# Kernel optimization log

Measured on AMD Instinct MI355X. Metric: run time of the kernel, lower is better.

## Reference

```python
import jax, jax.numpy as jnp
import numpy as np

B, N, D, H = 4, 2048, 1024, 16
DH = D // H


def setup_inputs() -> dict:
    key = jax.random.key(0)
    k_x, k_q, k_k, k_v, k_o = jax.random.split(key, 5)
    s = 1.0 / np.sqrt(D)
    return {
        "x": jax.random.normal(k_x, (B, N, D), dtype=jnp.float32),
        "mask": jnp.ones((B, N), dtype=bool),
        "Wq": jax.random.normal(k_q, (D, D), dtype=jnp.float32) * s,
        "Wk": jax.random.normal(k_k, (D, D), dtype=jnp.float32) * s,
        "Wv": jax.random.normal(k_v, (D, D), dtype=jnp.float32) * s,
        "Wo": jax.random.normal(k_o, (D, D), dtype=jnp.float32) * s,
    }


def reference(x, mask, Wq, Wk, Wv, Wo):
    # nn.Linear(bias=False): y = x @ W.T ; weights stored [out, in]
    q = jnp.einsum("bnd,ed->bne", x, Wq)
    k = jnp.einsum("bnd,ed->bne", x, Wk)
    v = jnp.einsum("bnd,ed->bne", x, Wv)
    # split heads: [b, n, d] -> [b, h, n, dh]
    def split(t):
        return t.reshape(B, N, H, DH).transpose(0, 2, 1, 3)
    q, k, v = split(q), split(k), split(v)
    # naive scaled dot-product attention (mask is dead code in the source)
    scores = jnp.einsum("bhnd,bhmd->bhnm", q, k) / jnp.sqrt(jnp.float32(DH))
    attn = jax.nn.softmax(scores, axis=-1)
    out = jnp.einsum("bhnm,bhmd->bhnd", attn, v)  # [b, h, n, dh]
    # merge heads: [b, h, n, dh] -> [b, n, d]
    out = out.transpose(0, 2, 1, 3).reshape(B, N, D)
    return jnp.einsum("bnd,ed->bne", out, Wo)
```

## Files before the change

### kernel.cpp

```cpp
#include <hip/hip_runtime.h>
#include <math.h>

constexpr int Bc  = 4;
constexpr int Nc  = 2048;
constexpr int Dc  = 1024;
constexpr int Hc  = 16;
constexpr int DHc = 64;
constexpr int Mrows = Bc * Nc;

typedef unsigned short ushortT;
typedef __attribute__((ext_vector_type(8))) short bf16x8;
typedef __attribute__((ext_vector_type(4))) unsigned short u16x4;
typedef __attribute__((ext_vector_type(4))) float f32x4;

#define QSCALE 0.18033688011112043f

#define GLD_LDS16(g, l)                                                        \
  __builtin_amdgcn_global_load_lds(                                            \
      (const __attribute__((address_space(1))) void*)(g),                      \
      (__attribute__((address_space(3))) void*)(l), 16, 0, 0)

__device__ inline ushortT f2bf(float f) {
  unsigned int u = __float_as_uint(f);
  u += 0x7fffu + ((u >> 16) & 1u);
  return (ushortT)(u >> 16);
}

__device__ inline float fexp2(float x) { return __builtin_amdgcn_exp2f(x); }

__global__ __launch_bounds__(256) void cvt_kernel(
    const float* __restrict__ x, const float* __restrict__ wq,
    const float* __restrict__ wk, const float* __restrict__ wv,
    const float* __restrict__ wo, ushortT* __restrict__ dst) {
  const int g = blockIdx.x * 256 + threadIdx.x;
  const float* src;
  size_t soff, doff;
  if (g < 2097152) {
    src = x;
    soff = (size_t)g * 4;
    doff = soff;
  } else {
    const int t = g - 2097152;
    const int w = t >> 18;
    const int off = t & 262143;
    src = (w == 0) ? wq : (w == 1) ? wk : (w == 2) ? wv : wo;
    soff = (size_t)off * 4;
    doff = 8388608u + (size_t)w * 1048576u + (size_t)off * 4;
  }
  float4 v = *(const float4*)(src + soff);
  ushort4 o = make_ushort4(f2bf(v.x), f2bf(v.y), f2bf(v.z), f2bf(v.w));
  *(ushort4*)(dst + doff) = o;
}

template <int QKV>
__global__ __launch_bounds__(256) void mfma_gemm(const ushortT* __restrict__ A,
                                                 const ushortT* __restrict__ W0,
                                                 void* __restrict__ C0) {
  __shared__ ushortT As[2][128 * 32];
  __shared__ ushortT Bs[2][128 * 32];

  const int tid = threadIdx.x;
  const int wave = tid >> 6, lane = tid & 63;
  const int quad = lane >> 4, lrow = lane & 15;

  const int gx = gridDim.x;
  const int nwg = gx * gridDim.y;
  const int orig = blockIdx.y * gx + blockIdx.x;
  const int swz = (orig & 7) * (nwg >> 3) + (orig >> 3);
  const int bx = swz % gx, by = swz / gx;

  const int wsel = QKV ? (bx >> 3) : 0;
  const int e0 = QKV ? ((bx & 7) * 128) : (bx * 128);
  const int m0 = by * 128;
  const ushortT* Wp = W0 + (size_t)wsel * (Dc * Dc);
  const float oscale = (QKV && wsel == 0) ? QSCALE : 1.0f;

  const ushortT* ag = A  + (size_t)(m0 + wave * 32 + (lane >> 2)) * Dc + (lane & 3) * 8;
  const ushortT* bg = Wp + (size_t)(e0 + wave * 32 + (lane >> 2)) * Dc + (lane & 3) * 8;
  const int lbase = wave * 1024 + lane * 8;

  f32x4 acc[4][4];
#pragma unroll
  for (int i = 0; i < 4; ++i)
#pragma unroll
    for (int j = 0; j < 4; ++j) acc[i][j] = (f32x4){0.f, 0.f, 0.f, 0.f};

  const int wm = (wave >> 1) * 64, wn = (wave & 1) * 64;

  for (int k0 = 0; k0 < Dc; k0 += 64) {
    __syncthreads();
#pragma unroll
    for (int p = 0; p < 2; ++p) {
      GLD_LDS16(ag + p * 32, &As[p][lbase]);
      GLD_LDS16(ag + p * 32 + 16 * Dc, &As[p][lbase + 512]);
      GLD_LDS16(bg + p * 32, &Bs[p][lbase]);
      GLD_LDS16(bg + p * 32 + 16 * Dc, &Bs[p][lbase + 512]);
    }
    ag += 64;
    bg += 64;
    __syncthreads();

#pragma unroll
    for (int p = 0; p < 2; ++p) {
      bf16x8 af[4], bf[4];
#pragma unroll
      for (int mt = 0; mt < 4; ++mt)
        af[mt] = *(const bf16x8*)(&As[p][(wm + mt * 16 + lrow) * 32 + quad * 8]);
#pragma unroll
      for (int nt = 0; nt < 4; ++nt)
        bf[nt] = *(const bf16x8*)(&Bs[p][(wn + nt * 16 + lrow) * 32 + quad * 8]);
      __builtin_amdgcn_s_setprio(1);
#pragma unroll
      for (int mt = 0; mt < 4; ++mt)
#pragma unroll
        for (int nt = 0; nt < 4; ++nt)
          acc[mt][nt] = __builtin_amdgcn_mfma_f32_16x16x32_bf16(
              af[mt], bf[nt], acc[mt][nt], 0, 0, 0);
      __builtin_amdgcn_s_setprio(0);
    }
  }

#pragma unroll
  for (int mt = 0; mt < 4; ++mt) {
#pragma unroll
    for (int nt = 0; nt < 4; ++nt) {
#pragma unroll
      for (int r = 0; r < 4; ++r) {
        const int m = m0 + wm + mt * 16 + quad * 4 + r;
        const int e = e0 + wn + nt * 16 + lrow;
        const float v = acc[mt][nt][r] * oscale;
        if (QKV) {
          const int b = m >> 11, n = m & 2047;
          const int h = e >> 6, dh = e & 63;
          ushortT* C = (ushortT*)C0 + (size_t)wsel * ((size_t)Mrows * Dc);
          C[(((size_t)(b * Hc + h)) * Nc + n) * DHc + dh] = f2bf(v);
        } else {
          ((float*)C0)[(size_t)m * Dc + e] = v;
        }
      }
    }
  }
}

__global__ __launch_bounds__(256, 2) void attn_mfma(const ushortT* __restrict__ Q,
                                                    const ushortT* __restrict__ K,
                                                    const ushortT* __restrict__ V,
                                                    ushortT* __restrict__ O) {
  __shared__ ushortT smemA[256 * 72];
  __shared__ ushortT Ks[2][64 * 64];
  __shared__ ushortT Vt[2][64 * 72];

  const int tid = threadIdx.x;
  const int wave = tid >> 6, lane = tid & 63;
  const int quad = lane >> 4, lrow = lane & 15;
  const int bh = blockIdx.y;
  const int q0 = blockIdx.x * 256;

  const ushortT* qg = Q + (size_t)bh * Nc * DHc;
  const ushortT* kg = K + (size_t)bh * Nc * DHc;
  const ushortT* vg = V + (size_t)bh * Nc * DHc;

  const int ksw = (lane & 3) ^ ((lane >> 3) & 3);
  const int krd = (lrow >> 1) & 3;

  const int kq = tid & 15;
  const int dhg = (tid >> 4) * 4;

#pragma unroll
  for (int c = 0; c < 2; ++c)
#pragma unroll
    for (int rh = 0; rh < 4; ++rh) {
      const int row = wave * 64 + rh * 16;
      GLD_LDS16(qg + (size_t)(q0 + row + (lane >> 2)) * DHc + c * 32 + (lane & 3) * 8,
                smemA + (c * 256 + row) * 32 + lane * 8);
    }
#pragma unroll
  for (int i = 0; i < 2; ++i) {
    const int cid = wave * 2 + i;
    const int c = cid & 1, kb = (cid >> 1) * 16;
    GLD_LDS16(kg + (size_t)(kb + (lane >> 2)) * DHc + c * 32 + ksw * 8,
              &Ks[0][(c * 64 + kb) * 32 + lane * 8]);
  }
  u16x4 vreg[4];
#pragma unroll
  for (int g = 0; g < 4; ++g)
    vreg[g] = *(const u16x4*)(vg + (size_t)(kq + 16 * g) * DHc + dhg);

  __syncthreads();

  bf16x8 af_q[4][2];
#pragma unroll
  for (int mt = 0; mt < 4; ++mt)
#pragma unroll
    for (int ks = 0; ks < 2; ++ks)
      af_q[mt][ks] = *(const bf16x8*)(smemA +
          ((ks * 256 + wave * 64 + mt * 16 + lrow) * 32 + quad * 8));

  {
    ushortT tmp[4][4];
#pragma unroll
    for (int g = 0; g < 4; ++g)
#pragma unroll
      for (int d = 0; d < 4; ++d) tmp[d][g] = vreg[g][d];
#pragma unroll
    for (int d = 0; d < 4; ++d)
      *(u16x4*)(&Vt[0][(dhg + d) * 72 + kq * 4]) = *(const u16x4*)tmp[d];
  }
  __syncthreads();

  f32x4 o_acc[4][4];
#pragma unroll
  for (int mt = 0; mt < 4; ++mt)
#pragma unroll
    for (int nt = 0; nt < 4; ++nt) o_acc[mt][nt] = (f32x4){0.f, 0.f, 0.f, 0.f};
  float l_i[16];
#pragma unroll
  for (int i = 0; i < 16; ++i) l_i[i] = 0.f;

  for (int k0 = 0; k0 < Nc; k0 += 64) {
    const int cur = (k0 >> 6) & 1, nxt = cur ^ 1;
    const bool pref = (k0 + 64 < Nc);

    if (pref) {
#pragma unroll
      for (int i = 0; i < 2; ++i) {
        const int cid = wave * 2 + i;
        const int c = cid & 1, kb = (cid >> 1) * 16;
        GLD_LDS16(kg + (size_t)(k0 + 64 + kb + (lane >> 2)) * DHc + c * 32 + ksw * 8,
                  &Ks[nxt][(c * 64 + kb) * 32 + lane * 8]);
      }
#pragma unroll
      for (int g = 0; g < 4; ++g)
        vreg[g] = *(const u16x4*)(vg + (size_t)(k0 + 64 + kq + 16 * g) * DHc + dhg);
    }

    bf16x8 bf_k[4][2];
#pragma unroll
    for (int nt = 0; nt < 4; ++nt)
#pragma unroll
      for (int ks = 0; ks < 2; ++ks)
        bf_k[nt][ks] = *(const bf16x8*)(
            &Ks[cur][(ks * 64 + nt * 16 + lrow) * 32 + (quad ^ krd) * 8]);

    f32x4 s_acc[4][4];
    __builtin_amdgcn_s_setprio(1);
#pragma unroll
    for (int mt = 0; mt < 4; ++mt)
#pragma unroll
      for (int nt = 0; nt < 4; ++nt) {
        s_acc[mt][nt] = (f32x4){0.f, 0.f, 0.f, 0.f};
#pragma unroll
        for (int ks = 0; ks < 2; ++ks)
          s_acc[mt][nt] = __builtin_amdgcn_mfma_f32_16x16x32_bf16(
              af_q[mt][ks], bf_k[nt][ks], s_acc[mt][nt], 0, 0, 0);
      }
    __builtin_amdgcn_s_setprio(0);

#pragma unroll
    for (int mt = 0; mt < 4; ++mt) {
#pragma unroll
      for (int r = 0; r < 4; ++r) {
        const float p0 = fexp2(s_acc[mt][0][r]);
        const float p1 = fexp2(s_acc[mt][1][r]);
        const float p2 = fexp2(s_acc[mt][2][r]);
        const float p3 = fexp2(s_acc[mt][3][r]);
        l_i[mt * 4 + r] += (p0 + p1) + (p2 + p3);
        const unsigned pk01 = __builtin_amdgcn_perm(
            __float_as_uint(p1), __float_as_uint(p0), 0x07060302u);
        const unsigned pk23 = __builtin_amdgcn_perm(
            __float_as_uint(p3), __float_as_uint(p2), 0x07060302u);
        const int row = wave * 64 + mt * 16 + quad * 4 + r;
        *(uint2*)(smemA + row * 72 + lrow * 4) = make_uint2(pk01, pk23);
      }
    }
    asm volatile("s_waitcnt lgkmcnt(0)" ::: "memory");

    bf16x8 af_p[4][2], bf_v[4][2];
#pragma unroll
    for (int mt = 0; mt < 4; ++mt)
#pragma unroll
      for (int ks = 0; ks < 2; ++ks)
        af_p[mt][ks] = *(const bf16x8*)(smemA +
            (wave * 64 + mt * 16 + lrow) * 72 + ks * 32 + quad * 8);
#pragma unroll
    for (int nt = 0; nt < 4; ++nt)
#pragma unroll
      for (int ks = 0; ks < 2; ++ks)
        bf_v[nt][ks] = *(const bf16x8*)(
            &Vt[cur][(nt * 16 + lrow) * 72 + ks * 32 + quad * 8]);
    __builtin_amdgcn_s_setprio(1);
#pragma unroll
    for (int mt = 0; mt < 4; ++mt)
#pragma unroll
      for (int nt = 0; nt < 4; ++nt)
#pragma unroll
        for (int ks = 0; ks < 2; ++ks)
          o_acc[mt][nt] = __builtin_amdgcn_mfma_f32_16x16x32_bf16(
              af_p[mt][ks], bf_v[nt][ks], o_acc[mt][nt], 0, 0, 0);
    __builtin_amdgcn_s_setprio(0);

    if (pref) {
      ushortT tmp[4][4];
#pragma unroll
      for (int g = 0; g < 4; ++g)
#pragma unroll
        for (int d = 0; d < 4; ++d) tmp[d][g] = vreg[g][d];
#pragma unroll
      for (int d = 0; d < 4; ++d)
        *(u16x4*)(&Vt[nxt][(dhg + d) * 72 + kq * 4]) = *(const u16x4*)tmp[d];
    }

    __syncthreads();
  }

#pragma unroll
  for (int i = 0; i < 16; ++i) {
    float s = l_i[i];
#pragma unroll
    for (int off = 8; off >= 1; off >>= 1) s += __shfl_xor(s, off, 16);
    l_i[i] = s;
  }

  const int b = bh / Hc, h = bh % Hc;
#pragma unroll
  for (int mt = 0; mt < 4; ++mt) {
#pragma unroll
    for (int r = 0; r < 4; ++r) {
      const float inv_l = 1.0f / l_i[mt * 4 + r];
      const int n = q0 + wave * 64 + mt * 16 + quad * 4 + r;
      const size_t base = ((size_t)b * Nc + n) * Dc + h * DHc;
#pragma unroll
      for (int nt = 0; nt < 4; ++nt)
        O[base + nt * 16 + lrow] = f2bf(o_acc[mt][nt][r] * inv_l);
    }
  }
}

extern "C" void kernel_launch(void* const* d_in, const int* in_sizes, int n_in,
                              void* d_out, int out_size, void* d_ws,
                              size_t ws_size, hipStream_t stream) {
  const float* x  = (const float*)d_in[0];
  const float* Wq = (const float*)d_in[2];
  const float* Wk = (const float*)d_in[3];
  const float* Wv = (const float*)d_in[4];
  const float* Wo = (const float*)d_in[5];

  ushortT* ws16 = (ushortT*)d_ws;
  ushortT* xb   = ws16;
  ushortT* wqb  = xb + (size_t)Mrows * Dc;
  ushortT* qkvb = wqb + 4 * (size_t)Dc * Dc;
  ushortT* qb   = qkvb;
  ushortT* kb   = qb + (size_t)Mrows * Dc;
  ushortT* vb   = kb + (size_t)Mrows * Dc;
  ushortT* aob  = vb + (size_t)Mrows * Dc;
  ushortT* wob  = wqb + 3 * (size_t)Dc * Dc;

  dim3 blk(256);
  hipLaunchKernelGGL(cvt_kernel, dim3(12288), blk, 0, stream, x, Wq, Wk, Wv, Wo,
                     ws16);

  hipLaunchKernelGGL((mfma_gemm<1>), dim3(24, Mrows / 128), blk, 0, stream, xb,
                     wqb, (void*)qkvb);

  hipLaunchKernelGGL(attn_mfma, dim3(Nc / 256, Bc * Hc), blk, 0, stream, qb,
                     kb, vb, aob);

  hipLaunchKernelGGL((mfma_gemm<0>), dim3(8, Mrows / 128), blk, 0, stream, aob,
                     wob, d_out);
}
```

Baseline: 297.6 us.

## Software-pipeline attention loop so next-tile QK^T overlaps current softmax and PV

Restructures the attention main loop into a two-stage software pipeline. The QK^T MFMAs for tile t+1 are issued while the exp/pack and PV MFMAs for tile t are in flight, using ping-pong score registers and a K prefetch two tiles ahead. V goes to a single-buffered LDS tile, which needs an extra barrier per iteration, and the setprio hints are dropped in both the GEMM and attention kernels. The aim is to hide exp and LDS latency behind matrix work, at the cost of more live registers (two score sets), which could cause spills or lower occupancy.

Result: slower. 524.6 us (+76.2%).

```diff
diff --git a/kernel.cpp b/kernel.cpp
--- a/kernel.cpp
+++ b/kernel.cpp
@@ -109,14 +109,12 @@
 #pragma unroll
       for (int nt = 0; nt < 4; ++nt)
         bf[nt] = *(const bf16x8*)(&Bs[p][(wn + nt * 16 + lrow) * 32 + quad * 8]);
-      __builtin_amdgcn_s_setprio(1);
 #pragma unroll
       for (int mt = 0; mt < 4; ++mt)
 #pragma unroll
         for (int nt = 0; nt < 4; ++nt)
           acc[mt][nt] = __builtin_amdgcn_mfma_f32_16x16x32_bf16(
               af[mt], bf[nt], acc[mt][nt], 0, 0, 0);
-      __builtin_amdgcn_s_setprio(0);
     }
   }
 
@@ -148,7 +146,7 @@
                                                     ushortT* __restrict__ O) {
   __shared__ ushortT smemA[256 * 72];
   __shared__ ushortT Ks[2][64 * 64];
-  __shared__ ushortT Vt[2][64 * 72];
+  __shared__ ushortT Vt[64 * 72];
 
   const int tid = threadIdx.x;
   const int wave = tid >> 6, lane = tid & 63;
@@ -204,10 +202,23 @@
       for (int d = 0; d < 4; ++d) tmp[d][g] = vreg[g][d];
 #pragma unroll
     for (int d = 0; d < 4; ++d)
-      *(u16x4*)(&Vt[0][(dhg + d) * 72 + kq * 4]) = *(const u16x4*)tmp[d];
-  }
+      *(u16x4*)(&Vt[(dhg + d) * 72 + kq * 4]) = *(const u16x4*)tmp[d];
+  }
+
+#pragma unroll
+  for (int g = 0; g < 4; ++g)
+    vreg[g] = *(const u16x4*)(vg + (size_t)(64 + kq + 16 * g) * DHc + dhg);
+#pragma unroll
+  for (int i = 0; i < 2; ++i) {
+    const int cid = wave * 2 + i;
+    const int c = cid & 1, kb = (cid >> 1) * 16;
+    GLD_LDS16(kg + (size_t)(64 + kb + (lane >> 2)) * DHc + c * 32 + ksw * 8,
+              &Ks[1][(c * 64 + kb) * 32 + lane * 8]);
+  }
+
   __syncthreads();
 
+  f32x4 sA[4][4], sB[4][4];
   f32x4 o_acc[4][4];
 #pragma unroll
   for (int mt = 0; mt < 4; ++mt)
@@ -217,64 +228,128 @@
 #pragma unroll
   for (int i = 0; i < 16; ++i) l_i[i] = 0.f;
 
-  for (int k0 = 0; k0 < Nc; k0 += 64) {
-    const int cur = (k0 >> 6) & 1, nxt = cur ^ 1;
-    const bool pref = (k0 + 64 < Nc);
-
-    if (pref) {
-#pragma unroll
-      for (int i = 0; i < 2; ++i) {
-        const int cid = wave * 2 + i;
-        const int c = cid & 1, kb = (cid >> 1) * 16;
-        GLD_LDS16(kg + (size_t)(k0 + 64 + kb + (lane >> 2)) * DHc + c * 32 + ksw * 8,
-                  &Ks[nxt][(c * 64 + kb) * 32 + lane * 8]);
-      }
-#pragma unroll
-      for (int g = 0; g < 4; ++g)
-        vreg[g] = *(const u16x4*)(vg + (size_t)(k0 + 64 + kq + 16 * g) * DHc + dhg);
-    }
-
+  {
     bf16x8 bf_k[4][2];
 #pragma unroll
     for (int nt = 0; nt < 4; ++nt)
 #pragma unroll
       for (int ks = 0; ks < 2; ++ks)
         bf_k[nt][ks] = *(const bf16x8*)(
-            &Ks[cur][(ks * 64 + nt * 16 + lrow) * 32 + (quad ^ krd) * 8]);
-
-    f32x4 s_acc[4][4];
-    __builtin_amdgcn_s_setprio(1);
+            &Ks[0][(ks * 64 + nt * 16 + lrow) * 32 + (quad ^ krd) * 8]);
 #pragma unroll
     for (int mt = 0; mt < 4; ++mt)
 #pragma unroll
       for (int nt = 0; nt < 4; ++nt) {
-        s_acc[mt][nt] = (f32x4){0.f, 0.f, 0.f, 0.f};
+        sA[mt][nt] = (f32x4){0.f, 0.f, 0.f, 0.f};
 #pragma unroll
         for (int ks = 0; ks < 2; ++ks)
-          s_acc[mt][nt] = __builtin_amdgcn_mfma_f32_16x16x32_bf16(
-              af_q[mt][ks], bf_k[nt][ks], s_acc[mt][nt], 0, 0, 0);
+          sA[mt][nt] = __builtin_amdgcn_mfma_f32_16x16x32_bf16(
+              af_q[mt][ks], bf_k[nt][ks], sA[mt][nt], 0, 0, 0);
       }
-    __builtin_amdgcn_s_setprio(0);
-
-#pragma unroll
-    for (int mt = 0; mt < 4; ++mt) {
-#pragma unroll
-      for (int r = 0; r < 4; ++r) {
-        const float p0 = fexp2(s_acc[mt][0][r]);
-        const float p1 = fexp2(s_acc[mt][1][r]);
-        const float p2 = fexp2(s_acc[mt][2][r]);
-        const float p3 = fexp2(s_acc[mt][3][r]);
-        l_i[mt * 4 + r] += (p0 + p1) + (p2 + p3);
-        const unsigned pk01 = __builtin_amdgcn_perm(
-            __float_as_uint(p1), __float_as_uint(p0), 0x07060302u);
-        const unsigned pk23 = __builtin_amdgcn_perm(
-            __float_as_uint(p3), __float_as_uint(p2), 0x07060302u);
-        const int row = wave * 64 + mt * 16 + quad * 4 + r;
-        *(uint2*)(smemA + row * 72 + lrow * 4) = make_uint2(pk01, pk23);
-      }
-    }
-    asm volatile("s_waitcnt lgkmcnt(0)" ::: "memory");
-
+  }
+  __syncthreads();
+
+#define BODY(T, CUR, SIN, SOUT, PREF1, PREF2)                                  \
+  {                                                                            \
+    const int k0b = (T) * 64;                                                  \
+    if (PREF1) {                                                               \
+      _Pragma("unroll") for (int g = 0; g < 4; ++g)                            \
+          vreg[g] = *(const u16x4*)(vg +                                       \
+              (size_t)(k0b + 64 + kq + 16 * g) * DHc + dhg);                   \
+    }                                                                          \
+    if (PREF2) {                                                               \
+      _Pragma("unroll") for (int i = 0; i < 2; ++i) {                          \
+        const int cid = wave * 2 + i;                                          \
+        const int cc = cid & 1, kb = (cid >> 1) * 16;                          \
+        GLD_LDS16(kg + (size_t)(k0b + 128 + kb + (lane >> 2)) * DHc +          \
+                      cc * 32 + ksw * 8,                                       \
+                  &Ks[CUR][(cc * 64 + kb) * 32 + lane * 8]);                   \
+      }                                                                        \
+    }                                                                          \
+    _Pragma("unroll") for (int mt = 0; mt < 4; ++mt) {                         \
+      _Pragma("unroll") for (int r = 0; r < 4; ++r) {                          \
+        const float p0 = fexp2(SIN[mt][0][r]);                                 \
+        const float p1 = fexp2(SIN[mt][1][r]);                                 \
+        const float p2 = fexp2(SIN[mt][2][r]);                                 \
+        const float p3 = fexp2(SIN[mt][3][r]);                                 \
+        l_i[mt * 4 + r] += (p0 + p1) + (p2 + p3);                              \
+        const unsigned pk01 = __builtin_amdgcn_perm(                           \
+            __float_as_uint(p1), __float_as_uint(p0), 0x07060302u);            \
+        const unsigned pk23 = __builtin_amdgcn_perm(                           \
+            __float_as_uint(p3), __float_as_uint(p2), 0x07060302u);            \
+        const int prow = wave * 64 + mt * 16 + quad * 4 + r;                   \
+        *(uint2*)(smemA + prow * 72 + lrow * 4) = make_uint2(pk01, pk23);      \
+      }                                                                        \
+    }                                                                          \
+    if (PREF1) {                                                               \
+      bf16x8 bf_k[4][2];                                                       \
+      _Pragma("unroll") for (int nt = 0; nt < 4; ++nt)                         \
+        _Pragma("unroll") for (int ks = 0; ks < 2; ++ks)                       \
+            bf_k[nt][ks] = *(const bf16x8*)(                                   \
+                &Ks[(CUR) ^ 1][(ks * 64 + nt * 16 + lrow) * 32 +               \
+                               (quad ^ krd) * 8]);                             \
+      _Pragma("unroll") for (int mt = 0; mt < 4; ++mt)                         \
+        _Pragma("unroll") for (int nt = 0; nt < 4; ++nt) {                     \
+          SOUT[mt][nt] = (f32x4){0.f, 0.f, 0.f, 0.f};                          \
+          _Pragma("unroll") for (int ks = 0; ks < 2; ++ks)                     \
+              SOUT[mt][nt] = __builtin_amdgcn_mfma_f32_16x16x32_bf16(          \
+                  af_q[mt][ks], bf_k[nt][ks], SOUT[mt][nt], 0, 0, 0);          \
+        }                                                                      \
+    }                                                                          \
+    asm volatile("s_waitcnt lgkmcnt(0)" ::: "memory");                         \
+    {                                                                          \
+      bf16x8 af_p[4][2], bf_v[4][2];                                           \
+      _Pragma("unroll") for (int mt = 0; mt < 4; ++mt)                         \
+        _Pragma("unroll") for (int ks = 0; ks < 2; ++ks)                       \
+            af_p[mt][ks] = *(const bf16x8*)(smemA +                            \
+                (wave * 64 + mt * 16 + lrow) * 72 + ks * 32 + quad * 8);       \
+      _Pragma("unroll") for (int nt = 0; nt < 4; ++nt)                         \
+        _Pragma("unroll") for (int ks = 0; ks < 2; ++ks)                       \
+            bf_v[nt][ks] = *(const bf16x8*)(                                   \
+                &Vt[(nt * 16 + lrow) * 72 + ks * 32 + quad * 8]);              \
+      _Pragma("unroll") for (int mt = 0; mt < 4; ++mt)                         \
+        _Pragma("unroll") for (int nt = 0; nt < 4; ++nt)                       \
+          _Pragma("unroll") for (int ks = 0; ks < 2; ++ks)                     \
+              o_acc[mt][nt] = __builtin_amdgcn_mfma_f32_16x16x32_bf16(         \
+                  af_p[mt][ks], bf_v[nt][ks], o_acc[mt][nt], 0, 0, 0);         \
+    }                                                                          \
+    __syncthreads();          \
+    if (PREF1) {                                                               \
+      ushortT tmp[4][4];                                                       \
+      _Pragma("unroll") for (int g = 0; g < 4; ++g)                            \
+        _Pragma("unroll") for (int d = 0; d < 4; ++d) tmp[d][g] = vreg[g][d];  \
+      _Pragma("unroll") for (int d = 0; d < 4; ++d)                            \
+          *(u16x4*)(&Vt[(dhg + d) * 72 + kq * 4]) = *(const u16x4*)tmp[d];     \
+    }                                                                          \
+    __syncthreads();         \
+  }
+
+#pragma unroll 1
+  for (int it = 0; it < 15; ++it) {
+    BODY(2 * it,     0, sA, sB, true, true)
+    BODY(2 * it + 1, 1, sB, sA, true, true)
+  }
+  BODY(30, 0, sA, sB, true, false)
+
+#pragma unroll
+  for (int mt = 0; mt < 4; ++mt) {
+#pragma unroll
+    for (int r = 0; r < 4; ++r) {
+      const float p0 = fexp2(sB[mt][0][r]);
+      const float p1 = fexp2(sB[mt][1][r]);
+      const float p2 = fexp2(sB[mt][2][r]);
+      const float p3 = fexp2(sB[mt][3][r]);
+      l_i[mt * 4 + r] += (p0 + p1) + (p2 + p3);
+      const unsigned pk01 = __builtin_amdgcn_perm(
+          __float_as_uint(p1), __float_as_uint(p0), 0x07060302u);
+      const unsigned pk23 = __builtin_amdgcn_perm(
+          __float_as_uint(p3), __float_as_uint(p2), 0x07060302u);
+      const int prow = wave * 64 + mt * 16 + quad * 4 + r;
+      *(uint2*)(smemA + prow * 72 + lrow * 4) = make_uint2(pk01, pk23);
+    }
+  }
+  asm volatile("s_waitcnt lgkmcnt(0)" ::: "memory");
+  {
     bf16x8 af_p[4][2], bf_v[4][2];
 #pragma unroll
     for (int mt = 0; mt < 4; ++mt)
@@ -287,8 +362,7 @@
 #pragma unroll
       for (int ks = 0; ks < 2; ++ks)
         bf_v[nt][ks] = *(const bf16x8*)(
-            &Vt[cur][(nt * 16 + lrow) * 72 + ks * 32 + quad * 8]);
-    __builtin_amdgcn_s_setprio(1);
+            &Vt[(nt * 16 + lrow) * 72 + ks * 32 + quad * 8]);
 #pragma unroll
     for (int mt = 0; mt < 4; ++mt)
 #pragma unroll
@@ -297,20 +371,6 @@
         for (int ks = 0; ks < 2; ++ks)
           o_acc[mt][nt] = __builtin_amdgcn_mfma_f32_16x16x32_bf16(
               af_p[mt][ks], bf_v[nt][ks], o_acc[mt][nt], 0, 0, 0);
-    __builtin_amdgcn_s_setprio(0);
-
-    if (pref) {
-      ushortT tmp[4][4];
-#pragma unroll
-      for (int g = 0; g < 4; ++g)
-#pragma unroll
-        for (int d = 0; d < 4; ++d) tmp[d][g] = vreg[g][d];
-#pragma unroll
-      for (int d = 0; d < 4; ++d)
-        *(u16x4*)(&Vt[nxt][(dhg + d) * 72 + kq * 4]) = *(const u16x4*)tmp[d];
-    }
-
-    __syncthreads();
   }
 
 #pragma unroll
```

## Software-pipeline attention loop so PV of previous tile overlaps QK and softmax

Applied to the files above, without the earlier changes.

Restructures the attention inner loop into a templated body that computes QK^T for tile T while doing the P·V MFMAs for tile T-1, keeping the previous P fragments in registers. The loop is unrolled by two with compile-time buffer indices, and a prologue and epilogue handle the first and last tiles. The aim is to hide the exp and LDS round-trip latency behind MFMA work. It also drops the s_setprio hints in both the GEMM and attention kernels, and the extra live P registers may raise register pressure.

Measured after the change: 498.9 us. +67.6%, slower.

```diff
diff --git a/kernel.cpp b/kernel.cpp
--- a/kernel.cpp
+++ b/kernel.cpp
@@ -109,14 +109,12 @@
 #pragma unroll
       for (int nt = 0; nt < 4; ++nt)
         bf[nt] = *(const bf16x8*)(&Bs[p][(wn + nt * 16 + lrow) * 32 + quad * 8]);
-      __builtin_amdgcn_s_setprio(1);
 #pragma unroll
       for (int mt = 0; mt < 4; ++mt)
 #pragma unroll
         for (int nt = 0; nt < 4; ++nt)
           acc[mt][nt] = __builtin_amdgcn_mfma_f32_16x16x32_bf16(
               af[mt], bf[nt], acc[mt][nt], 0, 0, 0);
-      __builtin_amdgcn_s_setprio(0);
     }
   }
 
@@ -142,6 +140,106 @@
   }
 }
 
+__device__ __forceinline__ f32x4 MFMA(bf16x8 a, bf16x8 b, f32x4 c) {
+  return __builtin_amdgcn_mfma_f32_16x16x32_bf16(a, b, c, 0, 0, 0);
+}
+
+template <int KC, bool PVON, bool PREF>
+__device__ __forceinline__ void attn_body(
+    int T, const ushortT* __restrict__ kg, const ushortT* __restrict__ vg,
+    ushortT* smemA, ushortT (&Ks)[2][64 * 64], ushortT (&Vt)[2][64 * 72],
+    const bf16x8 (&af_q)[4][2], bf16x8 (&af_pH)[4][2], u16x4 (&vreg)[4],
+    f32x4 (&o_acc)[4][4], float (&l_i)[16], int wave, int lane, int quad,
+    int lrow, int ksw, int krd, int kq, int dhg) {
+  const int k0b = T * 64;
+
+  if (PREF) {
+#pragma unroll
+    for (int i = 0; i < 2; ++i) {
+      const int cid = wave * 2 + i;
+      const int c = cid & 1, kb = (cid >> 1) * 16;
+      GLD_LDS16(kg + (size_t)(k0b + 64 + kb + (lane >> 2)) * DHc + c * 32 + ksw * 8,
+                &Ks[KC ^ 1][(c * 64 + kb) * 32 + lane * 8]);
+    }
+#pragma unroll
+    for (int g = 0; g < 4; ++g)
+      vreg[g] = *(const u16x4*)(vg + (size_t)(k0b + 64 + kq + 16 * g) * DHc + dhg);
+  }
+
+  bf16x8 bf_k[4][2];
+#pragma unroll
+  for (int nt = 0; nt < 4; ++nt)
+#pragma unroll
+    for (int ks = 0; ks < 2; ++ks)
+      bf_k[nt][ks] = *(const bf16x8*)(
+          &Ks[KC][(ks * 64 + nt * 16 + lrow) * 32 + (quad ^ krd) * 8]);
+  f32x4 s_acc[4][4];
+#pragma unroll
+  for (int mt = 0; mt < 4; ++mt)
+#pragma unroll
+    for (int nt = 0; nt < 4; ++nt) {
+      s_acc[mt][nt] = (f32x4){0.f, 0.f, 0.f, 0.f};
+#pragma unroll
+      for (int ks = 0; ks < 2; ++ks)
+        s_acc[mt][nt] = MFMA(af_q[mt][ks], bf_k[nt][ks], s_acc[mt][nt]);
+    }
+
+  if (PVON) {
+    bf16x8 bf_v[4][2];
+#pragma unroll
+    for (int nt = 0; nt < 4; ++nt)
+#pragma unroll
+      for (int ks = 0; ks < 2; ++ks)
+        bf_v[nt][ks] = *(const bf16x8*)(
+            &Vt[KC ^ 1][(nt * 16 + lrow) * 72 + ks * 32 + quad * 8]);
+#pragma unroll
+    for (int mt = 0; mt < 4; ++mt)
+#pragma unroll
+      for (int nt = 0; nt < 4; ++nt)
+#pragma unroll
+        for (int ks = 0; ks < 2; ++ks)
+          o_acc[mt][nt] = MFMA(af_pH[mt][ks], bf_v[nt][ks], o_acc[mt][nt]);
+  }
+
+#pragma unroll
+  for (int mt = 0; mt < 4; ++mt) {
+#pragma unroll
+    for (int r = 0; r < 4; ++r) {
+      const float p0 = fexp2(s_acc[mt][0][r]);
+      const float p1 = fexp2(s_acc[mt][1][r]);
+      const float p2 = fexp2(s_acc[mt][2][r]);
+      const float p3 = fexp2(s_acc[mt][3][r]);
+      l_i[mt * 4 + r] += (p0 + p1) + (p2 + p3);
+      const unsigned pk01 = __builtin_amdgcn_perm(
+          __float_as_uint(p1), __float_as_uint(p0), 0x07060302u);
+      const unsigned pk23 = __builtin_amdgcn_perm(
+          __float_as_uint(p3), __float_as_uint(p2), 0x07060302u);
+      const int prow = wave * 64 + mt * 16 + quad * 4 + r;
+      *(uint2*)(smemA + prow * 72 + lrow * 4) = make_uint2(pk01, pk23);
+    }
+  }
+  asm volatile("s_waitcnt lgkmcnt(0)" ::: "memory");
+#pragma unroll
+  for (int mt = 0; mt < 4; ++mt)
+#pragma unroll
+    for (int ks = 0; ks < 2; ++ks)
+      af_pH[mt][ks] = *(const bf16x8*)(smemA +
+          (wave * 64 + mt * 16 + lrow) * 72 + ks * 32 + quad * 8);
+
+  __syncthreads();
+
+  if (PREF) {
+    ushortT tmp[4][4];
+#pragma unroll
+    for (int g = 0; g < 4; ++g)
+#pragma unroll
+      for (int d = 0; d < 4; ++d) tmp[d][g] = vreg[g][d];
+#pragma unroll
+    for (int d = 0; d < 4; ++d)
+      *(u16x4*)(&Vt[KC ^ 1][(dhg + d) * 72 + kq * 4]) = *(const u16x4*)tmp[d];
+  }
+}
+
 __global__ __launch_bounds__(256, 2) void attn_mfma(const ushortT* __restrict__ Q,
                                                     const ushortT* __restrict__ K,
                                                     const ushortT* __restrict__ V,
@@ -208,6 +306,7 @@
   }
   __syncthreads();
 
+  bf16x8 af_pH[4][2];
   f32x4 o_acc[4][4];
 #pragma unroll
   for (int mt = 0; mt < 4; ++mt)
@@ -217,100 +316,33 @@
 #pragma unroll
   for (int i = 0; i < 16; ++i) l_i[i] = 0.f;
 
-  for (int k0 = 0; k0 < Nc; k0 += 64) {
-    const int cur = (k0 >> 6) & 1, nxt = cur ^ 1;
-    const bool pref = (k0 + 64 < Nc);
-
-    if (pref) {
-#pragma unroll
-      for (int i = 0; i < 2; ++i) {
-        const int cid = wave * 2 + i;
-        const int c = cid & 1, kb = (cid >> 1) * 16;
-        GLD_LDS16(kg + (size_t)(k0 + 64 + kb + (lane >> 2)) * DHc + c * 32 + ksw * 8,
-                  &Ks[nxt][(c * 64 + kb) * 32 + lane * 8]);
-      }
-#pragma unroll
-      for (int g = 0; g < 4; ++g)
-        vreg[g] = *(const u16x4*)(vg + (size_t)(k0 + 64 + kq + 16 * g) * DHc + dhg);
-    }
-
-    bf16x8 bf_k[4][2];
-#pragma unroll
-    for (int nt = 0; nt < 4; ++nt)
-#pragma unroll
-      for (int ks = 0; ks < 2; ++ks)
-        bf_k[nt][ks] = *(const bf16x8*)(
-            &Ks[cur][(ks * 64 + nt * 16 + lrow) * 32 + (quad ^ krd) * 8]);
-
-    f32x4 s_acc[4][4];
-    __builtin_amdgcn_s_setprio(1);
-#pragma unroll
-    for (int mt = 0; mt < 4; ++mt)
-#pragma unroll
-      for (int nt = 0; nt < 4; ++nt) {
-        s_acc[mt][nt] = (f32x4){0.f, 0.f, 0.f, 0.f};
-#pragma unroll
-        for (int ks = 0; ks < 2; ++ks)
-          s_acc[mt][nt] = __builtin_amdgcn_mfma_f32_16x16x32_bf16(
-              af_q[mt][ks], bf_k[nt][ks], s_acc[mt][nt], 0, 0, 0);
-      }
-    __builtin_amdgcn_s_setprio(0);
-
-#pragma unroll
-    for (int mt = 0; mt < 4; ++mt) {
-#pragma unroll
-      for (int r = 0; r < 4; ++r) {
-        const float p0 = fexp2(s_acc[mt][0][r]);
-        const float p1 = fexp2(s_acc[mt][1][r]);
-        const float p2 = fexp2(s_acc[mt][2][r]);
-        const float p3 = fexp2(s_acc[mt][3][r]);
-        l_i[mt * 4 + r] += (p0 + p1) + (p2 + p3);
-        const unsigned pk01 = __builtin_amdgcn_perm(
-            __float_as_uint(p1), __float_as_uint(p0), 0x07060302u);
-        const unsigned pk23 = __builtin_amdgcn_perm(
-            __float_as_uint(p3), __float_as_uint(p2), 0x07060302u);
-        const int row = wave * 64 + mt * 16 + quad * 4 + r;
-        *(uint2*)(smemA + row * 72 + lrow * 4) = make_uint2(pk01, pk23);
-      }
-    }
-    asm volatile("s_waitcnt lgkmcnt(0)" ::: "memory");
-
-    bf16x8 af_p[4][2], bf_v[4][2];
-#pragma unroll
-    for (int mt = 0; mt < 4; ++mt)
-#pragma unroll
-      for (int ks = 0; ks < 2; ++ks)
-        af_p[mt][ks] = *(const bf16x8*)(smemA +
-            (wave * 64 + mt * 16 + lrow) * 72 + ks * 32 + quad * 8);
+  attn_body<0, false, true>(0, kg, vg, smemA, Ks, Vt, af_q, af_pH, vreg,
+                            o_acc, l_i, wave, lane, quad, lrow, ksw, krd, kq, dhg);
+#pragma unroll 1
+  for (int it = 0; it < 15; ++it) {
+    attn_body<1, true, true>(1 + 2 * it, kg, vg, smemA, Ks, Vt, af_q, af_pH,
+                             vreg, o_acc, l_i, wave, lane, quad, lrow, ksw, krd, kq, dhg);
+    attn_body<0, true, true>(2 + 2 * it, kg, vg, smemA, Ks, Vt, af_q, af_pH,
+                             vreg, o_acc, l_i, wave, lane, quad, lrow, ksw, krd, kq, dhg);
+  }
+  attn_body<1, true, false>(31, kg, vg, smemA, Ks, Vt, af_q, af_pH, vreg,
+                            o_acc, l_i, wave, lane, quad, lrow, ksw, krd, kq, dhg);
+
+  {
+    bf16x8 bf_v[4][2];
 #pragma unroll
     for (int nt = 0; nt < 4; ++nt)
 #pragma unroll
       for (int ks = 0; ks < 2; ++ks)
         bf_v[nt][ks] = *(const bf16x8*)(
-            &Vt[cur][(nt * 16 + lrow) * 72 + ks * 32 + quad * 8]);
-    __builtin_amdgcn_s_setprio(1);
+            &Vt[1][(nt * 16 + lrow) * 72 + ks * 32 + quad * 8]);
 #pragma unroll
     for (int mt = 0; mt < 4; ++mt)
 #pragma unroll
       for (int nt = 0; nt < 4; ++nt)
 #pragma unroll
         for (int ks = 0; ks < 2; ++ks)
-          o_acc[mt][nt] = __builtin_amdgcn_mfma_f32_16x16x32_bf16(
-              af_p[mt][ks], bf_v[nt][ks], o_acc[mt][nt], 0, 0, 0);
-    __builtin_amdgcn_s_setprio(0);
-
-    if (pref) {
-      ushortT tmp[4][4];
-#pragma unroll
-      for (int g = 0; g < 4; ++g)
-#pragma unroll
-        for (int d = 0; d < 4; ++d) tmp[d][g] = vreg[g][d];
-#pragma unroll
-      for (int d = 0; d < 4; ++d)
-        *(u16x4*)(&Vt[nxt][(dhg + d) * 72 + kq * 4]) = *(const u16x4*)tmp[d];
-    }
-
-    __syncthreads();
+          o_acc[mt][nt] = MFMA(af_pH[mt][ks], bf_v[nt][ks], o_acc[mt][nt]);
   }
 
 #pragma unroll
```
